# Kernel optimization log

Hardware: AMD Instinct MI355X
Metric: run time of the kernel (lower is better)

The kernel has to match this reference:

```python
import jax, jax.numpy as jnp
import numpy as np

B, S, H = 4, 512, 768
D, M = 24, 96          # hdim_proj_dim, hdim_mlp_hidden
O = 2 * max(128, H // 2)  # val_mlp hidden = 768


def setup_inputs() -> dict:
    key = jax.random.key(0)
    ks = jax.random.split(key, 14)
    u = lambda k, shp, fan_in: jax.random.uniform(k, shp, jnp.float32, -1.0, 1.0) / np.float32(np.sqrt(fan_in))
    return {
        'H_j': jax.random.normal(ks[0], (B, S, H), jnp.float32),
        'H_i': jax.random.normal(ks[1], (B, S, H), jnp.float32),
        'Wpj': u(ks[2], (H, D), H),
        'Wpi': u(ks[3], (H, D), H),
        'Ws1': u(ks[4], (4 * D, M), 4 * D),
        'bs1': u(ks[5], (M,), 4 * D),
        'ws2': u(ks[6], (M,), M),
        'bs2': u(ks[7], (), M),
        'Wv1': u(ks[8], (3 * H, O), 3 * H),
        'bv1': u(ks[9], (O,), 3 * H),
        'Wv2': u(ks[10], (O, H), O),
        'bv2': u(ks[11], (H,), O),
        'alpha': jnp.float32(0.05),
        'attn_mask': jnp.ones((B, S), jnp.int32),
    }


def reference(H_j, H_i, Wpj, Wpi, Ws1, bs1, ws2, bs2, Wv1, bv1, Wv2, bv2, alpha, attn_mask):
    # Projections [B,S,D]
    Zj = H_j @ Wpj
    Zi = H_i @ Wpi
    # 4term score MLP, first layer decomposed over the concat blocks:
    # cat(Zj_p, Zi_p, Zj_p*Zi_p, |Zj_p - Zi_p|) @ Ws1
    W1j, W1i, W1h, W1d = Ws1[:D], Ws1[D:2 * D], Ws1[2 * D:3 * D], Ws1[3 * D:]
    tj = Zj @ W1j                                   # [B,P,M]
    ti = Zi @ W1i                                   # [B,Q,M]
    th = jnp.einsum('bpd,bqd,dm->bpqm', Zj, Zi, W1h)  # hadamard term
    diff = jnp.abs(Zj[:, :, None, :] - Zi[:, None, :, :])  # [B,P,Q,D]
    td = jnp.einsum('bpqd,dm->bpqm', diff, W1d)
    hid = jax.nn.relu(tj[:, :, None, :] + ti[:, None, :, :] + th + td + bs1)  # [B,P,Q,M]
    logits = jnp.einsum('bpqm,m->bpq', hid, ws2) + bs2  # [B,P,Q]
    # mask over source tokens (last dim); token_temp == 1.0 so no division
    mask = attn_mask.astype(logits.dtype)
    logits = logits + (1.0 - mask)[:, None, :] * jnp.finfo(logits.dtype).min
    probs = jax.nn.softmax(logits, axis=-1)
    ctx = jnp.einsum('bpq,bqh->bph', probs, H_i)    # [B,S,H]
    # val_mlp on cat(ctx, H_j, ctx*H_j), first layer decomposed
    Wc, Wj, Wh = Wv1[:H], Wv1[H:2 * H], Wv1[2 * H:]
    mhid = jax.nn.relu(ctx @ Wc + H_j @ Wj + (ctx * H_j) @ Wh + bv1)
    msg = mhid @ Wv2 + bv2
    # dropout is identity in eval mode
    return alpha * msg
```

## Files before the change

### kernel.cpp

```cpp
#include <hip/hip_runtime.h>
#include <hip/hip_bf16.h>

#define Bb 4
#define Ss 512
#define Hh 768
#define Dd 24
#define Mm 96
#define Oo 768

typedef __bf16 bf16x8 __attribute__((ext_vector_type(8)));
typedef float f32x4 __attribute__((ext_vector_type(4)));

__device__ __forceinline__ void transpose_tile(
    const float* __restrict__ s, __bf16* __restrict__ d,
    int R, int C, int bx, int by, float* smem, int tid)
{
    const int x = tid & 31, y = tid >> 5;
    const int c0 = bx * 32, r0 = by * 32;
    #pragma unroll
    for (int i = 0; i < 4; ++i)
        smem[(y + 8 * i) * 33 + x] = s[(size_t)(r0 + y + 8 * i) * C + c0 + x];
    __syncthreads();
    #pragma unroll
    for (int i = 0; i < 4; ++i)
        d[(size_t)(c0 + y + 8 * i) * R + r0 + x] = (__bf16)smem[x * 33 + (y + 8 * i)];
}

__global__ __launch_bounds__(256) void prep_kernel(
    const float* __restrict__ Hj, const float* __restrict__ Hi,
    const float* __restrict__ Wpj, const float* __restrict__ Wpi,
    const float* __restrict__ Wv1, const float* __restrict__ Wv2,
    float* __restrict__ Zj, float* __restrict__ Zi,
    __bf16* __restrict__ HiT, __bf16* __restrict__ Wv1T,
    __bf16* __restrict__ Wv2T, __bf16* __restrict__ Acat)
{
    __shared__ float smem[1088];
    const int bid = blockIdx.x;
    const int tid = threadIdx.x;

    if (bid < 4096) {
        const int row = bid & 2047;
        const int which = bid >> 11;
        const float* src = (which ? Hi : Hj) + (size_t)row * Hh;
        const float* W = which ? Wpi : Wpj;
        float* Z = which ? Zi : Zj;
        float* rowbuf = smem;
        float* partial = smem + 768;
        for (int i = tid; i < Hh; i += 256) rowbuf[i] = src[i];
        __syncthreads();
        if (tid < 192) {
            const int d = tid % Dd;
            const int c = tid / Dd;
            const int h0 = c * 96;
            float s = 0.f;
            #pragma unroll 4
            for (int h = h0; h < h0 + 96; ++h) s = fmaf(rowbuf[h], W[h * Dd + d], s);
            partial[c * Dd + d] = s;
        }
        __syncthreads();
        if (tid < Dd) {
            float s = 0.f;
            #pragma unroll
            for (int c = 0; c < 8; ++c) s += partial[c * Dd + tid];
            Z[(size_t)row * Dd + tid] = s;
        }
    } else if (bid < 5632) {
        int rem = bid - 4096;
        const int bz = rem / 384; rem %= 384;
        transpose_tile(Hi + (size_t)bz * Ss * Hh, HiT + (size_t)bz * Hh * Ss,
                       Ss, Hh, rem % 24, rem / 24, smem, tid);
    } else if (bid < 7360) {
        const int rem = bid - 5632;
        transpose_tile(Wv1, Wv1T, 3 * Hh, Oo, rem % 24, rem / 24, smem, tid);
    } else if (bid < 7936) {
        const int rem = bid - 7360;
        transpose_tile(Wv2, Wv2T, Oo, Hh, rem % 24, rem / 24, smem, tid);
    } else {
        const int idx = (bid - 7936) * 256 + tid;
        const int row = idx / 96, c8 = idx % 96;
        const float* s = Hj + (size_t)row * Hh + c8 * 8;
        const float4 u = *(const float4*)s;
        const float4 v = *(const float4*)(s + 4);
        bf16x8 o;
        o[0]=(__bf16)u.x; o[1]=(__bf16)u.y; o[2]=(__bf16)u.z; o[3]=(__bf16)u.w;
        o[4]=(__bf16)v.x; o[5]=(__bf16)v.y; o[6]=(__bf16)v.z; o[7]=(__bf16)v.w;
        *(bf16x8*)&Acat[(size_t)row * 2304 + Hh + c8 * 8] = o;
    }
}

__global__ __launch_bounds__(256) void pair_kernel(
    const float* __restrict__ Zj, const float* __restrict__ Zi,
    const float* __restrict__ Ws1, const float* __restrict__ bs1,
    const float* __restrict__ ws2, const float* __restrict__ bs2p,
    const int* __restrict__ mask, __bf16* __restrict__ probs)
{
    const int bp = blockIdx.x;
    const int b  = bp >> 9;
    const int tid  = threadIdx.x;
    const int lane = tid & 63;
    const int wid  = tid >> 6;
    const int col  = lane & 15;
    const int g    = lane >> 4;

    __shared__ float zjall[Dd];
    __shared__ float rowadd[Mm];
    __shared__ float logitsl[Ss];
    __shared__ float red[8];

    if (tid < Dd) zjall[tid] = Zj[(size_t)bp * Dd + tid];
    __syncthreads();
    if (tid < Mm) {
        float s = bs1[tid];
        #pragma unroll
        for (int d = 0; d < Dd; ++d) s = fmaf(zjall[d], Ws1[d * Mm + tid], s);
        rowadd[tid] = s;
    }
    __syncthreads();

    float zj8[8];
    if (g < 3) {
        const float* zr = Zj + (size_t)bp * Dd + g * 8;
        const float4 u = *(const float4*)zr;
        const float4 v = *(const float4*)(zr + 4);
        zj8[0]=u.x; zj8[1]=u.y; zj8[2]=u.z; zj8[3]=u.w;
        zj8[4]=v.x; zj8[5]=v.y; zj8[6]=v.z; zj8[7]=v.w;
    } else {
        #pragma unroll
        for (int j = 0; j < 8; ++j) zj8[j] = 0.f;
    }

    bf16x8 bw[6][2];
    float ws2r[6];
    #pragma unroll
    for (int n = 0; n < 6; ++n) {
        const int m = n * 16 + col;
        ws2r[n] = ws2[m];
        bf16x8 b0, b1;
        if (g < 3) {
            #pragma unroll
            for (int j = 0; j < 8; ++j) {
                const int d = g * 8 + j;
                b0[j] = (__bf16)(fmaf(zj8[j], Ws1[(2 * Dd + d) * Mm + m],
                                      Ws1[(Dd + d) * Mm + m]));
                b1[j] = (__bf16)(Ws1[(3 * Dd + d) * Mm + m]);
            }
        } else {
            #pragma unroll
            for (int j = 0; j < 8; ++j) { b0[j] = (__bf16)0.f; b1[j] = (__bf16)0.f; }
            b0[0] = (__bf16)rowadd[m];
        }
        bw[n][0] = b0; bw[n][1] = b1;
    }

    const float* zib = Zi + (size_t)b * Ss * Dd;

    #pragma unroll 2
    for (int t = 0; t < 8; ++t) {
        const int q0 = wid * 128 + t * 16;
        bf16x8 a0, a1;
        if (g < 3) {
            const float* zr = zib + (size_t)(q0 + col) * Dd + g * 8;
            const float4 u = *(const float4*)zr;
            const float4 v = *(const float4*)(zr + 4);
            a0[0]=(__bf16)u.x; a0[1]=(__bf16)u.y; a0[2]=(__bf16)u.z; a0[3]=(__bf16)u.w;
            a0[4]=(__bf16)v.x; a0[5]=(__bf16)v.y; a0[6]=(__bf16)v.z; a0[7]=(__bf16)v.w;
            a1[0]=(__bf16)fabsf(zj8[0]-u.x); a1[1]=(__bf16)fabsf(zj8[1]-u.y);
            a1[2]=(__bf16)fabsf(zj8[2]-u.z); a1[3]=(__bf16)fabsf(zj8[3]-u.w);
            a1[4]=(__bf16)fabsf(zj8[4]-v.x); a1[5]=(__bf16)fabsf(zj8[5]-v.y);
            a1[6]=(__bf16)fabsf(zj8[6]-v.z); a1[7]=(__bf16)fabsf(zj8[7]-v.w);
        } else {
            #pragma unroll
            for (int j = 0; j < 8; ++j) { a0[j] = (__bf16)0.f; a1[j] = (__bf16)0.f; }
            a0[0] = (__bf16)1.0f;
        }

        f32x4 acc[6];
        #pragma unroll
        for (int n = 0; n < 6; ++n) acc[n] = (f32x4){0.f, 0.f, 0.f, 0.f};
        #pragma unroll
        for (int n = 0; n < 6; ++n) {
            acc[n] = __builtin_amdgcn_mfma_f32_16x16x32_bf16(a0, bw[n][0], acc[n], 0, 0, 0);
            acc[n] = __builtin_amdgcn_mfma_f32_16x16x32_bf16(a1, bw[n][1], acc[n], 0, 0, 0);
        }

        float lsum[4] = {0.f, 0.f, 0.f, 0.f};
        #pragma unroll
        for (int n = 0; n < 6; ++n)
            #pragma unroll
            for (int r = 0; r < 4; ++r)
                lsum[r] = fmaf(fmaxf(acc[n][r], 0.f), ws2r[n], lsum[r]);
        #pragma unroll
        for (int off = 1; off <= 8; off <<= 1) {
            #pragma unroll
            for (int r = 0; r < 4; ++r) lsum[r] += __shfl_xor(lsum[r], off);
        }
        if (col == 0) {
            float4 o = {lsum[0], lsum[1], lsum[2], lsum[3]};
            *(float4*)&logitsl[q0 + g * 4] = o;
        }
    }
    __syncthreads();

    const float bs2v = bs2p[0];
    const int* mrow = mask + (size_t)b * Ss;
    float l0 = logitsl[tid]       + bs2v + (1.0f - (float)mrow[tid])       * (-3.402823466e+38f);
    float l1 = logitsl[tid + 256] + bs2v + (1.0f - (float)mrow[tid + 256]) * (-3.402823466e+38f);
    float vmax = fmaxf(l0, l1);
    #pragma unroll
    for (int off = 32; off > 0; off >>= 1) vmax = fmaxf(vmax, __shfl_xor(vmax, off));
    if (lane == 0) red[wid] = vmax;
    __syncthreads();
    const float mx = fmaxf(fmaxf(red[0], red[1]), fmaxf(red[2], red[3]));
    const float e0 = __expf(l0 - mx);
    const float e1 = __expf(l1 - mx);
    float vs = e0 + e1;
    #pragma unroll
    for (int off = 32; off > 0; off >>= 1) vs += __shfl_xor(vs, off);
    if (lane == 0) red[4 + wid] = vs;
    __syncthreads();
    const float inv = 1.0f / (red[4] + red[5] + red[6] + red[7]);
    __bf16* prow = probs + (size_t)bp * Ss;
    prow[tid] = (__bf16)(e0 * inv);
    prow[tid + 256] = (__bf16)(e1 * inv);
}

__device__ __forceinline__ void gload16(const __bf16* g, __bf16* l)
{
    __builtin_amdgcn_global_load_lds(
        (const __attribute__((address_space(1))) void*)g,
        (__attribute__((address_space(3))) void*)l, 16, 0, 0);
}

__device__ __forceinline__ int swz(int row, int k)
{
    return row * 64 + (k ^ ((row & 7) << 3));
}

template<int MODE>
__global__ __launch_bounds__(256) void gemm_kernel(
    const __bf16* __restrict__ A, const __bf16* __restrict__ Bt,
    const float* __restrict__ Hjf, const float* __restrict__ bias,
    const float* __restrict__ alphap,
    __bf16* __restrict__ obf, float* __restrict__ of)
{
    constexpr int K = (MODE == 0) ? 512 : (MODE == 1) ? 2304 : 768;
    constexpr int NIT = K / 64;

    __shared__ __align__(16) __bf16 As[3][64 * 64];
    __shared__ __align__(16) __bf16 Bs[3][96 * 64];

    const int tid = threadIdx.x;
    const int lane = tid & 63;
    const int wid = tid >> 6;
    const int col = lane & 15, g = lane >> 4;
    const int wm = wid >> 1, wn = wid & 1;
    const int r0 = blockIdx.x * 64;
    const int n0 = blockIdx.y * 96;
    const __bf16* Btb = (MODE == 0) ? Bt + (size_t)(r0 >> 9) * (Hh * Ss) : Bt;

    const __bf16* asrc[2];
    const __bf16* bsrc[3];
    int aldo[2], bldo[3];
    #pragma unroll
    for (int i = 0; i < 2; ++i) {
        const int c = (wid * 2 + i) * 64 + lane;
        const int row = c >> 3;
        const int k16 = (c & 7) ^ (row & 7);
        asrc[i] = A + (size_t)(r0 + row) * K + k16 * 8;
        aldo[i] = (wid * 2 + i) * 512;
    }
    #pragma unroll
    for (int i = 0; i < 3; ++i) {
        const int c = (wid * 3 + i) * 64 + lane;
        const int row = c >> 3;
        const int k16 = (c & 7) ^ (row & 7);
        bsrc[i] = Btb + (size_t)(n0 + row) * K + k16 * 8;
        bldo[i] = (wid * 3 + i) * 512;
    }

    auto stage = [&](int t, int buf) {
        __bf16* ab = &As[buf][0];
        __bf16* bb = &Bs[buf][0];
        #pragma unroll
        for (int i = 0; i < 2; ++i) gload16(asrc[i] + (size_t)t * 64, ab + aldo[i]);
        #pragma unroll
        for (int i = 0; i < 3; ++i) gload16(bsrc[i] + (size_t)t * 64, bb + bldo[i]);
    };

    f32x4 acc[2][3];
    #pragma unroll
    for (int mi = 0; mi < 2; ++mi)
        #pragma unroll
        for (int ni = 0; ni < 3; ++ni) acc[mi][ni] = (f32x4){0.f, 0.f, 0.f, 0.f};

    stage(0, 0);
    stage(1, 1);

    for (int it = 0; it < NIT; ++it) {
        if (it < NIT - 1) asm volatile("s_waitcnt vmcnt(5)" ::: "memory");
        else              asm volatile("s_waitcnt vmcnt(0)" ::: "memory");
        __builtin_amdgcn_s_barrier();
        __builtin_amdgcn_sched_barrier(0);
        if (it + 2 < NIT) stage(it + 2, (it + 2) % 3);

        const __bf16* Ac = As[it % 3];
        const __bf16* Bc = Bs[it % 3];
        #pragma unroll
        for (int h = 0; h < 2; ++h) {
            const int ka = h * 32 + g * 8;
            const bf16x8 a0 = *(const bf16x8*)&Ac[swz(wm * 32 +      col, ka)];
            const bf16x8 a1 = *(const bf16x8*)&Ac[swz(wm * 32 + 16 + col, ka)];
            const bf16x8 b0 = *(const bf16x8*)&Bc[swz(wn * 48 +      col, ka)];
            const bf16x8 b1 = *(const bf16x8*)&Bc[swz(wn * 48 + 16 + col, ka)];
            const bf16x8 b2 = *(const bf16x8*)&Bc[swz(wn * 48 + 32 + col, ka)];
            acc[0][0] = __builtin_amdgcn_mfma_f32_16x16x32_bf16(a0, b0, acc[0][0], 0, 0, 0);
            acc[0][1] = __builtin_amdgcn_mfma_f32_16x16x32_bf16(a0, b1, acc[0][1], 0, 0, 0);
            acc[0][2] = __builtin_amdgcn_mfma_f32_16x16x32_bf16(a0, b2, acc[0][2], 0, 0, 0);
            acc[1][0] = __builtin_amdgcn_mfma_f32_16x16x32_bf16(a1, b0, acc[1][0], 0, 0, 0);
            acc[1][1] = __builtin_amdgcn_mfma_f32_16x16x32_bf16(a1, b1, acc[1][1], 0, 0, 0);
            acc[1][2] = __builtin_amdgcn_mfma_f32_16x16x32_bf16(a1, b2, acc[1][2], 0, 0, 0);
        }
    }

    const float al = (MODE == 2) ? alphap[0] : 0.f;
    #pragma unroll
    for (int mi = 0; mi < 2; ++mi) {
        #pragma unroll
        for (int r = 0; r < 4; ++r) {
            const int row = r0 + wm * 32 + mi * 16 + g * 4 + r;
            #pragma unroll
            for (int ni = 0; ni < 3; ++ni) {
                const int cn = n0 + wn * 48 + ni * 16 + col;
                const float v = acc[mi][ni][r];
                if (MODE == 0) {
                    const float hjv = Hjf[(size_t)row * Hh + cn];
                    obf[(size_t)row * 2304 + cn] = (__bf16)v;
                    obf[(size_t)row * 2304 + 1536 + cn] = (__bf16)(v * hjv);
                } else if (MODE == 1) {
                    obf[(size_t)row * Oo + cn] = (__bf16)fmaxf(v + bias[cn], 0.f);
                } else {
                    of[(size_t)row * Hh + cn] = al * (v + bias[cn]);
                }
            }
        }
    }
}

extern "C" void kernel_launch(void* const* d_in, const int* in_sizes, int n_in,
                              void* d_out, int out_size, void* d_ws, size_t ws_size,
                              hipStream_t stream)
{
    const float* Hj  = (const float*)d_in[0];
    const float* Hi  = (const float*)d_in[1];
    const float* Wpj = (const float*)d_in[2];
    const float* Wpi = (const float*)d_in[3];
    const float* Ws1 = (const float*)d_in[4];
    const float* bs1 = (const float*)d_in[5];
    const float* ws2 = (const float*)d_in[6];
    const float* bs2 = (const float*)d_in[7];
    const float* Wv1 = (const float*)d_in[8];
    const float* bv1 = (const float*)d_in[9];
    const float* Wv2 = (const float*)d_in[10];
    const float* bv2 = (const float*)d_in[11];
    const float* alpha = (const float*)d_in[12];
    const int* mask  = (const int*)d_in[13];

    float* ws = (float*)d_ws;
    float* Zj      = ws;
    float* Zi      = Zj + 49152;
    float* probs_f = Zi + 49152;
    float* HiT_f   = probs_f + 524288;
    float* Wv2T_f  = HiT_f + 786432;
    float* mhid_f  = Wv2T_f + 294912;
    float* Acat_f  = mhid_f + 786432;
    float* Wv1T_f  = Acat_f + 2359296;

    __bf16* probs_bf = (__bf16*)probs_f;
    __bf16* HiT      = (__bf16*)HiT_f;
    __bf16* Wv2T     = (__bf16*)Wv2T_f;
    __bf16* mhid_bf  = (__bf16*)mhid_f;
    __bf16* Acat     = (__bf16*)Acat_f;
    __bf16* Wv1T     = (__bf16*)Wv1T_f;

    prep_kernel<<<dim3(8704), 256, 0, stream>>>(
        Hj, Hi, Wpj, Wpi, Wv1, Wv2, Zj, Zi, HiT, Wv1T, Wv2T, Acat);
    pair_kernel<<<dim3(Bb * Ss), 256, 0, stream>>>(
        Zj, Zi, Ws1, bs1, ws2, bs2, mask, probs_bf);
    gemm_kernel<0><<<dim3(2048 / 64, Hh / 96), 256, 0, stream>>>(
        probs_bf, HiT, Hj, nullptr, nullptr, Acat, nullptr);
    gemm_kernel<1><<<dim3(2048 / 64, Oo / 96), 256, 0, stream>>>(
        Acat, Wv1T, nullptr, bv1, nullptr, mhid_bf, nullptr);
    gemm_kernel<2><<<dim3(2048 / 64, Hh / 96), 256, 0, stream>>>(
        mhid_bf, Wv2T, nullptr, bv2, alpha, nullptr, (float*)d_out);
}
```

Baseline: 191.6 us.

## Precompute packed bf16 MFMA operands in prep kernel for pair kernel

Moves the per-row B-operand construction (Zj-dependent hadamard/i weights plus the row bias term) and the shared difference-weight operand out of pair_kernel into prep_kernel. Both are written as padded 32-wide bf16 layouts, and Z tensors are padded to 32 with a ones column so pair_kernel loads MFMA fragments directly without branches or conversions. It also adds a launch_bounds occupancy hint. The cost is an extra ~6MB B0all workspace written and re-read per row, plus more global traffic in prep.

Measured after the change: 199.9 us. 4.3% more time.

```diff
diff --git a/kernel.cpp b/kernel.cpp
--- a/kernel.cpp
+++ b/kernel.cpp
@@ -30,7 +30,10 @@
     const float* __restrict__ Hj, const float* __restrict__ Hi,
     const float* __restrict__ Wpj, const float* __restrict__ Wpi,
     const float* __restrict__ Wv1, const float* __restrict__ Wv2,
-    float* __restrict__ Zj, float* __restrict__ Zi,
+    const float* __restrict__ Ws1, const float* __restrict__ bs1,
+    float* __restrict__ Zj_pad, float* __restrict__ Zi_pad,
+    __bf16* __restrict__ Zi_pack, __bf16* __restrict__ B0all,
+    __bf16* __restrict__ B1g,
     __bf16* __restrict__ HiT, __bf16* __restrict__ Wv1T,
     __bf16* __restrict__ Wv2T, __bf16* __restrict__ Acat)
 {
@@ -43,9 +46,9 @@
         const int which = bid >> 11;
         const float* src = (which ? Hi : Hj) + (size_t)row * Hh;
         const float* W = which ? Wpi : Wpj;
-        float* Z = which ? Zi : Zj;
         float* rowbuf = smem;
         float* partial = smem + 768;
+        float* zfin = smem + 960;
         for (int i = tid; i < Hh; i += 256) rowbuf[i] = src[i];
         __syncthreads();
         if (tid < 192) {
@@ -62,7 +65,34 @@
             float s = 0.f;
             #pragma unroll
             for (int c = 0; c < 8; ++c) s += partial[c * Dd + tid];
-            Z[(size_t)row * Dd + tid] = s;
+            zfin[tid] = s;
+        }
+        __syncthreads();
+        if (tid < 32) {
+            const float v = (tid < Dd) ? zfin[tid] : 0.f;
+            float* Zp = which ? Zi_pad : Zj_pad;
+            Zp[(size_t)row * 32 + tid] = v;
+            if (which)
+                Zi_pack[(size_t)row * 32 + tid] =
+                    (__bf16)((tid < Dd) ? v : (tid == Dd ? 1.f : 0.f));
+        }
+        if (!which && tid < Mm) {
+            const int m = tid;
+            float ra = bs1[m];
+            #pragma unroll
+            for (int d = 0; d < Dd; ++d) ra = fmaf(zfin[d], Ws1[d * Mm + m], ra);
+            __bf16 outv[32];
+            #pragma unroll
+            for (int d = 0; d < Dd; ++d)
+                outv[d] = (__bf16)fmaf(zfin[d], Ws1[(2 * Dd + d) * Mm + m],
+                                       Ws1[(Dd + d) * Mm + m]);
+            outv[Dd] = (__bf16)ra;
+            #pragma unroll
+            for (int k = Dd + 1; k < 32; ++k) outv[k] = (__bf16)0.f;
+            __bf16* dst = B0all + ((size_t)row * Mm + m) * 32;
+            #pragma unroll
+            for (int k = 0; k < 4; ++k)
+                *(bf16x8*)(dst + k * 8) = *(bf16x8*)&outv[k * 8];
         }
     } else if (bid < 5632) {
         int rem = bid - 4096;
@@ -75,7 +105,7 @@
     } else if (bid < 7936) {
         const int rem = bid - 7360;
         transpose_tile(Wv2, Wv2T, Oo, Hh, rem % 24, rem / 24, smem, tid);
-    } else {
+    } else if (bid < 8704) {
         const int idx = (bid - 7936) * 256 + tid;
         const int row = idx / 96, c8 = idx % 96;
         const float* s = Hj + (size_t)row * Hh + c8 * 8;
@@ -85,12 +115,27 @@
         o[0]=(__bf16)u.x; o[1]=(__bf16)u.y; o[2]=(__bf16)u.z; o[3]=(__bf16)u.w;
         o[4]=(__bf16)v.x; o[5]=(__bf16)v.y; o[6]=(__bf16)v.z; o[7]=(__bf16)v.w;
         *(bf16x8*)&Acat[(size_t)row * 2304 + Hh + c8 * 8] = o;
-    }
-}
-
-__global__ __launch_bounds__(256) void pair_kernel(
-    const float* __restrict__ Zj, const float* __restrict__ Zi,
-    const float* __restrict__ Ws1, const float* __restrict__ bs1,
+    } else {
+        if (tid < Mm) {
+            const int m = tid;
+            __bf16 outv[32];
+            #pragma unroll
+            for (int d = 0; d < Dd; ++d)
+                outv[d] = (__bf16)Ws1[(3 * Dd + d) * Mm + m];
+            #pragma unroll
+            for (int k = Dd; k < 32; ++k) outv[k] = (__bf16)0.f;
+            __bf16* dst = B1g + (size_t)m * 32;
+            #pragma unroll
+            for (int k = 0; k < 4; ++k)
+                *(bf16x8*)(dst + k * 8) = *(bf16x8*)&outv[k * 8];
+        }
+    }
+}
+
+__global__ __launch_bounds__(256, 4) void pair_kernel(
+    const float* __restrict__ Zj_pad, const float* __restrict__ Zi_pad,
+    const __bf16* __restrict__ Zi_pack, const __bf16* __restrict__ B0all,
+    const __bf16* __restrict__ B1g,
     const float* __restrict__ ws2, const float* __restrict__ bs2p,
     const int* __restrict__ mask, __bf16* __restrict__ probs)
 {
@@ -102,85 +147,52 @@
     const int col  = lane & 15;
     const int g    = lane >> 4;
 
-    __shared__ float zjall[Dd];
-    __shared__ float rowadd[Mm];
     __shared__ float logitsl[Ss];
     __shared__ float red[8];
 
-    if (tid < Dd) zjall[tid] = Zj[(size_t)bp * Dd + tid];
-    __syncthreads();
-    if (tid < Mm) {
-        float s = bs1[tid];
-        #pragma unroll
-        for (int d = 0; d < Dd; ++d) s = fmaf(zjall[d], Ws1[d * Mm + tid], s);
-        rowadd[tid] = s;
-    }
-    __syncthreads();
-
     float zj8[8];
-    if (g < 3) {
-        const float* zr = Zj + (size_t)bp * Dd + g * 8;
+    {
+        const float* zr = Zj_pad + (size_t)bp * 32 + g * 8;
         const float4 u = *(const float4*)zr;
         const float4 v = *(const float4*)(zr + 4);
         zj8[0]=u.x; zj8[1]=u.y; zj8[2]=u.z; zj8[3]=u.w;
         zj8[4]=v.x; zj8[5]=v.y; zj8[6]=v.z; zj8[7]=v.w;
-    } else {
-        #pragma unroll
-        for (int j = 0; j < 8; ++j) zj8[j] = 0.f;
-    }
-
-    bf16x8 bw[6][2];
+    }
+
+    bf16x8 bw0[6], bw1[6];
     float ws2r[6];
+    const __bf16* b0base = B0all + (size_t)bp * Mm * 32;
     #pragma unroll
     for (int n = 0; n < 6; ++n) {
         const int m = n * 16 + col;
         ws2r[n] = ws2[m];
-        bf16x8 b0, b1;
-        if (g < 3) {
-            #pragma unroll
-            for (int j = 0; j < 8; ++j) {
-                const int d = g * 8 + j;
-                b0[j] = (__bf16)(fmaf(zj8[j], Ws1[(2 * Dd + d) * Mm + m],
-                                      Ws1[(Dd + d) * Mm + m]));
-                b1[j] = (__bf16)(Ws1[(3 * Dd + d) * Mm + m]);
-            }
-        } else {
-            #pragma unroll
-            for (int j = 0; j < 8; ++j) { b0[j] = (__bf16)0.f; b1[j] = (__bf16)0.f; }
-            b0[0] = (__bf16)rowadd[m];
-        }
-        bw[n][0] = b0; bw[n][1] = b1;
-    }
-
-    const float* zib = Zi + (size_t)b * Ss * Dd;
+        bw0[n] = *(const bf16x8*)(b0base + (size_t)m * 32 + g * 8);
+        bw1[n] = *(const bf16x8*)(B1g + (size_t)m * 32 + g * 8);
+    }
+
+    const float*  zipb = Zi_pad  + (size_t)b * Ss * 32;
+    const __bf16* zpkb = Zi_pack + (size_t)b * Ss * 32;
 
     #pragma unroll 2
     for (int t = 0; t < 8; ++t) {
         const int q0 = wid * 128 + t * 16;
-        bf16x8 a0, a1;
-        if (g < 3) {
-            const float* zr = zib + (size_t)(q0 + col) * Dd + g * 8;
-            const float4 u = *(const float4*)zr;
-            const float4 v = *(const float4*)(zr + 4);
-            a0[0]=(__bf16)u.x; a0[1]=(__bf16)u.y; a0[2]=(__bf16)u.z; a0[3]=(__bf16)u.w;
-            a0[4]=(__bf16)v.x; a0[5]=(__bf16)v.y; a0[6]=(__bf16)v.z; a0[7]=(__bf16)v.w;
-            a1[0]=(__bf16)fabsf(zj8[0]-u.x); a1[1]=(__bf16)fabsf(zj8[1]-u.y);
-            a1[2]=(__bf16)fabsf(zj8[2]-u.z); a1[3]=(__bf16)fabsf(zj8[3]-u.w);
-            a1[4]=(__bf16)fabsf(zj8[4]-v.x); a1[5]=(__bf16)fabsf(zj8[5]-v.y);
-            a1[6]=(__bf16)fabsf(zj8[6]-v.z); a1[7]=(__bf16)fabsf(zj8[7]-v.w);
-        } else {
-            #pragma unroll
-            for (int j = 0; j < 8; ++j) { a0[j] = (__bf16)0.f; a1[j] = (__bf16)0.f; }
-            a0[0] = (__bf16)1.0f;
-        }
+        const int q  = q0 + col;
+        const bf16x8 a0 = *(const bf16x8*)(zpkb + (size_t)q * 32 + g * 8);
+        const float4 u = *(const float4*)(zipb + (size_t)q * 32 + g * 8);
+        const float4 v = *(const float4*)(zipb + (size_t)q * 32 + g * 8 + 4);
+        bf16x8 a1;
+        a1[0]=(__bf16)fabsf(zj8[0]-u.x); a1[1]=(__bf16)fabsf(zj8[1]-u.y);
+        a1[2]=(__bf16)fabsf(zj8[2]-u.z); a1[3]=(__bf16)fabsf(zj8[3]-u.w);
+        a1[4]=(__bf16)fabsf(zj8[4]-v.x); a1[5]=(__bf16)fabsf(zj8[5]-v.y);
+        a1[6]=(__bf16)fabsf(zj8[6]-v.z); a1[7]=(__bf16)fabsf(zj8[7]-v.w);
 
         f32x4 acc[6];
         #pragma unroll
         for (int n = 0; n < 6; ++n) acc[n] = (f32x4){0.f, 0.f, 0.f, 0.f};
         #pragma unroll
         for (int n = 0; n < 6; ++n) {
-            acc[n] = __builtin_amdgcn_mfma_f32_16x16x32_bf16(a0, bw[n][0], acc[n], 0, 0, 0);
-            acc[n] = __builtin_amdgcn_mfma_f32_16x16x32_bf16(a1, bw[n][1], acc[n], 0, 0, 0);
+            acc[n] = __builtin_amdgcn_mfma_f32_16x16x32_bf16(a0, bw0[n], acc[n], 0, 0, 0);
+            acc[n] = __builtin_amdgcn_mfma_f32_16x16x32_bf16(a1, bw1[n], acc[n], 0, 0, 0);
         }
 
         float lsum[4] = {0.f, 0.f, 0.f, 0.f};
@@ -366,15 +378,21 @@
     const int* mask  = (const int*)d_in[13];
 
     float* ws = (float*)d_ws;
-    float* Zj      = ws;
-    float* Zi      = Zj + 49152;
-    float* probs_f = Zi + 49152;
+    float* Zj_pad  = ws;
+    float* Zi_pad  = Zj_pad + 65536;
+    float* Zpack_f = Zi_pad + 65536;
+    float* B1_f    = Zpack_f + 32768;
+    float* B0_f    = B1_f + 1536;
+    float* probs_f = B0_f + 3145728;
     float* HiT_f   = probs_f + 524288;
     float* Wv2T_f  = HiT_f + 786432;
     float* mhid_f  = Wv2T_f + 294912;
     float* Acat_f  = mhid_f + 786432;
     float* Wv1T_f  = Acat_f + 2359296;
 
+    __bf16* Zi_pack  = (__bf16*)Zpack_f;
+    __bf16* B1g      = (__bf16*)B1_f;
+    __bf16* B0all    = (__bf16*)B0_f;
     __bf16* probs_bf = (__bf16*)probs_f;
     __bf16* HiT      = (__bf16*)HiT_f;
     __bf16* Wv2T     = (__bf16*)Wv2T_f;
@@ -382,10 +400,11 @@
     __bf16* Acat     = (__bf16*)Acat_f;
     __bf16* Wv1T     = (__bf16*)Wv1T_f;
 
-    prep_kernel<<<dim3(8704), 256, 0, stream>>>(
-        Hj, Hi, Wpj, Wpi, Wv1, Wv2, Zj, Zi, HiT, Wv1T, Wv2T, Acat);
+    prep_kernel<<<dim3(8705), 256, 0, stream>>>(
+        Hj, Hi, Wpj, Wpi, Wv1, Wv2, Ws1, bs1,
+        Zj_pad, Zi_pad, Zi_pack, B0all, B1g, HiT, Wv1T, Wv2T, Acat);
     pair_kernel<<<dim3(Bb * Ss), 256, 0, stream>>>(
-        Zj, Zi, Ws1, bs1, ws2, bs2, mask, probs_bf);
+        Zj_pad, Zi_pad, Zi_pack, B0all, B1g, ws2, bs2, mask, probs_bf);
     gemm_kernel<0><<<dim3(2048 / 64, Hh / 96), 256, 0, stream>>>(
         probs_bf, HiT, Hj, nullptr, nullptr, Acat, nullptr);
     gemm_kernel<1><<<dim3(2048 / 64, Oo / 96), 256, 0, stream>>>(
```
